# Kernel tuning notes

Measured on AMD Instinct MI355X. Metric: run time of the kernel, lower is better.

## Reference

```python
import jax, jax.numpy as jnp
import numpy as np

N_NODES = 100000
N_EDGES = 1600000
D = 128


def setup_inputs() -> dict:
    key = jax.random.key(0)
    ks = jax.random.split(key, 9)
    inp = {
        "embs": jax.random.normal(ks[0], (N_NODES, D), dtype=jnp.float32),
        "edge_index0": jax.random.randint(ks[1], (2, N_EDGES), 0, N_NODES, dtype=jnp.int64 if jax.config.jax_enable_x64 else jnp.int32),
        "edge_index1": jax.random.randint(ks[2], (2, N_EDGES), 0, N_NODES, dtype=jnp.int64 if jax.config.jax_enable_x64 else jnp.int32),
        "w_l0": jax.random.normal(ks[3], (D, D), dtype=jnp.float32) * (1.0 / np.sqrt(D)),
        "w_r0": jax.random.normal(ks[4], (D, D), dtype=jnp.float32) * (1.0 / np.sqrt(D)),
        "b0": jnp.zeros((D,), dtype=jnp.float32),
        "w_l1": jax.random.normal(ks[5], (D, D), dtype=jnp.float32) * (1.0 / np.sqrt(D)),
        "w_r1": jax.random.normal(ks[6], (D, D), dtype=jnp.float32) * (1.0 / np.sqrt(D)),
        "b1": jnp.zeros((D,), dtype=jnp.float32),
    }
    return inp


def _sage_conv(x, edge_index, w_l, w_r, b):
    # PyG SAGEConv: out[i] = lin_l(mean_{j->i} x[j]) + lin_r(x[i])
    src, dst = edge_index[0], edge_index[1]
    n = x.shape[0]
    msg = jnp.take(x, src, axis=0)                                  # [E, D] gather
    summed = jax.ops.segment_sum(msg, dst, num_segments=n)          # [N, D] scatter-add
    cnt = jax.ops.segment_sum(jnp.ones(src.shape, x.dtype), dst, num_segments=n)
    agg = summed / jnp.maximum(cnt, 1.0)[:, None]                   # mean; 0 for isolated nodes
    return agg @ w_l.T + b + x @ w_r.T


def reference(embs, edge_index0, edge_index1, w_l0, w_r0, b0, w_l1, w_r1, b1):
    # layer 0 (not last): dropout (eval -> identity) + GELU (torch default = exact erf)
    x = _sage_conv(embs, edge_index0, w_l0, w_r0, b0)
    x = jax.nn.gelu(x, approximate=False)
    # layer 1 (last): no dropout / activation
    x = _sage_conv(x, edge_index1, w_l1, w_r1, b1)
    return x
```

## Files before the change

### kernel.cpp

```cpp
#include <hip/hip_runtime.h>
#include <hip/hip_fp16.h>
#include <math.h>

#define D 128
#define SH 9
#define BW (1 << SH)
#define EPT 16

typedef _Float16 half4v __attribute__((ext_vector_type(4)));
typedef _Float16 half8  __attribute__((ext_vector_type(8)));
typedef float    floatx16 __attribute__((ext_vector_type(16)));

__global__ __launch_bounds__(256) void cast_half(
        const float* __restrict__ x, _Float16* __restrict__ y, int n) {
    int i = blockIdx.x * 256 + threadIdx.x;
    int idx = i * 4;
    if (idx >= n) return;
    float4 v = *(const float4*)(x + idx);
    half4v h;
    h[0] = (_Float16)v.x; h[1] = (_Float16)v.y;
    h[2] = (_Float16)v.z; h[3] = (_Float16)v.w;
    *(half4v*)(y + idx) = h;
}

__global__ __launch_bounds__(256) void prep_bswz(
        const float* __restrict__ wl, const float* __restrict__ wr,
        _Float16* __restrict__ B) {
    int idx = blockIdx.x * 256 + threadIdx.x;
    if (idx >= 64 * 512) return;
    int j = idx & 7;
    int lane = (idx >> 3) & 63;
    int f = idx >> 9;
    int ks = f >> 2, cb = f & 3;
    int k = ks * 16 + (lane >> 5) * 8 + j;
    int c = cb * 32 + (lane & 31);
    float v = (k < 128) ? wl[c * 128 + k] : wr[c * 128 + (k - 128)];
    B[idx] = (_Float16)v;
}

__global__ __launch_bounds__(256) void hist_coarse(
        const int* __restrict__ ei0, const int* __restrict__ ei1,
        int E, int NBK, int* __restrict__ ccnt) {
    __shared__ int h[512];
    int NBIN = 2 * NBK;
    int t = threadIdx.x;
    h[t] = 0; h[t + 256] = 0;
    __syncthreads();
    int t0 = blockIdx.x * (256 * EPT) + t;
#pragma unroll
    for (int k = 0; k < EPT; ++k) {
        int idx = t0 + k * 256;
        if (idx < 2 * E) {
            int g = idx >= E;
            int e = idx - g * E;
            int dst = (g ? ei1 : ei0)[E + e];
            atomicAdd(&h[g * NBK + (dst >> SH)], 1);
        }
    }
    __syncthreads();
    for (int b = t; b < NBIN; b += 256)
        if (h[b]) atomicAdd(&ccnt[b * 16], h[b]);
}

__global__ __launch_bounds__(256) void scan_coarse(
        const int* __restrict__ ccnt, int NBK, int E, int N,
        int* __restrict__ gbase, int* __restrict__ gcur,
        int* __restrict__ rp0, int* __restrict__ rp1) {
    __shared__ int part[256];
    int t = threadIdx.x;
    for (int g = 0; g < 2; ++g) {
        int v = (t < NBK) ? ccnt[(g * NBK + t) * 16] : 0;
        part[t] = v;
        __syncthreads();
        for (int off = 1; off < 256; off <<= 1) {
            int u = (t >= off) ? part[t - off] : 0;
            __syncthreads();
            part[t] += u;
            __syncthreads();
        }
        if (t < NBK) {
            int ex = (t == 0) ? 0 : part[t - 1];
            int b = g * NBK + t;
            gbase[b] = ex;
            gcur[b * 16] = ex;
        }
        __syncthreads();
    }
    if (t == 0) { rp0[N] = E; rp1[N] = E; }
}

__global__ __launch_bounds__(256) void bin_pass1(
        const int* __restrict__ ei0, const int* __restrict__ ei1,
        int E, int NBK, int* __restrict__ gcur,
        int* __restrict__ stage0, int* __restrict__ stage1) {
    __shared__ int cnt[512];
    __shared__ int base[512];
    int NBIN = 2 * NBK;
    int t = threadIdx.x;
    cnt[t] = 0; cnt[t + 256] = 0;
    __syncthreads();
    int t0 = blockIdx.x * (256 * EPT) + t;
    int pk[EPT];
    int bn[EPT];
#pragma unroll
    for (int k = 0; k < EPT; ++k) {
        int idx = t0 + k * 256;
        bn[k] = -1;
        if (idx < 2 * E) {
            int g = idx >= E;
            int e = idx - g * E;
            const int* ei = g ? ei1 : ei0;
            int src = ei[e];
            int dst = ei[E + e];
            pk[k] = src | ((dst & (BW - 1)) << 17);
            bn[k] = g * NBK + (dst >> SH);
            atomicAdd(&cnt[bn[k]], 1);
        }
    }
    __syncthreads();
    for (int b = t; b < NBIN; b += 256) {
        int c = cnt[b];
        base[b] = c ? atomicAdd(&gcur[b * 16], c) : 0;
        cnt[b] = 0;
    }
    __syncthreads();
#pragma unroll
    for (int k = 0; k < EPT; ++k) {
        if (bn[k] >= 0) {
            int b = bn[k];
            int r = atomicAdd(&cnt[b], 1);
            int* stage = (b >= NBK) ? stage1 : stage0;
            stage[base[b] + r] = pk[k];
        }
    }
}

__global__ __launch_bounds__(256) void bin_pass2(
        const int* __restrict__ gbase,
        const int* __restrict__ stage0, const int* __restrict__ stage1,
        int* __restrict__ rp0, int* __restrict__ rp1,
        int* __restrict__ es0, int* __restrict__ es1,
        int N, int NBK, int E) {
    __shared__ int cnt[BW];
    __shared__ int part[256];
    int b = blockIdx.x;
    int g = b >= NBK;
    int bk = b - g * NBK;
    const int* stage = g ? stage1 : stage0;
    int* rp = g ? rp1 : rp0;
    int* es = g ? es1 : es0;
    int lo = bk << SH;
    int hi = min(lo + BW, N);
    int nd = hi - lo;
    int beg = gbase[b];
    int end = (bk == NBK - 1) ? E : gbase[b + 1];
    int t = threadIdx.x;
    cnt[t] = 0; cnt[t + 256] = 0;
    __syncthreads();
    for (int i = beg + t; i < end; i += 256)
        atomicAdd(&cnt[(unsigned)stage[i] >> 17], 1);
    __syncthreads();
    int c0 = cnt[t * 2], c1 = cnt[t * 2 + 1];
    part[t] = c0 + c1;
    __syncthreads();
    for (int off = 1; off < 256; off <<= 1) {
        int u = (t >= off) ? part[t - off] : 0;
        __syncthreads();
        part[t] += u;
        __syncthreads();
    }
    int ex = (t == 0) ? 0 : part[t - 1];
    int base0 = beg + ex;
    if (t * 2 < nd)     rp[lo + t * 2]     = base0;
    if (t * 2 + 1 < nd) rp[lo + t * 2 + 1] = base0 + c0;
    __syncthreads();
    cnt[t * 2] = base0;
    cnt[t * 2 + 1] = base0 + c0;
    __syncthreads();
    int i = beg + t;
    for (; i + 768 < end; i += 1024) {
        unsigned p0 = (unsigned)stage[i];
        unsigned p1 = (unsigned)stage[i + 256];
        unsigned p2 = (unsigned)stage[i + 512];
        unsigned p3 = (unsigned)stage[i + 768];
        int q0 = atomicAdd(&cnt[p0 >> 17], 1);
        int q1 = atomicAdd(&cnt[p1 >> 17], 1);
        int q2 = atomicAdd(&cnt[p2 >> 17], 1);
        int q3 = atomicAdd(&cnt[p3 >> 17], 1);
        es[q0] = p0 & 0x1FFFF;
        es[q1] = p1 & 0x1FFFF;
        es[q2] = p2 & 0x1FFFF;
        es[q3] = p3 & 0x1FFFF;
    }
    for (; i < end; i += 256) {
        unsigned p = (unsigned)stage[i];
        int q = atomicAdd(&cnt[p >> 17], 1);
        es[q] = p & 0x1FFFF;
    }
}

__global__ __launch_bounds__(256) void agg_half(
        const _Float16* __restrict__ x, const int* __restrict__ row_ptr,
        const int* __restrict__ edge_src, _Float16* __restrict__ agg, int N) {
    int gt = blockIdx.x * 256 + threadIdx.x;
    int w = gt >> 6;
    int lane = gt & 63;
    if (w >= N) return;
    int beg = row_ptr[w];
    int end = row_ptr[w + 1];
    int grp = lane >> 5;
    int c   = lane & 31;
    unsigned co = (unsigned)c * 8u;
    const char* xb = (const char*)x;
    float ax = 0.f, ay = 0.f, az = 0.f, aw = 0.f;
    float one = 1.0f;

    for (int chunk = beg; chunk < end; chunk += 64) {
        int n = min(64, end - chunk);
        int iv = (lane < n) ? edge_src[chunk + lane] : -1;
        for (int e = 0; e < n; e += 8) {
            int s[4];
            uint2 v[4];
#pragma unroll
            for (int j = 0; j < 4; ++j)
                s[j] = __shfl(iv, e + 2 * j + grp);
#pragma unroll
            for (int j = 0; j < 4; ++j) {
                v[j] = make_uint2(0u, 0u);
                if (s[j] >= 0)
                    v[j] = *(const uint2*)(xb + (unsigned)s[j] * 256u + co);
            }
#pragma unroll
            for (int j = 0; j < 4; ++j) {
                asm("v_fma_mix_f32 %0, %1, %2, %0 op_sel:[0,0,0] op_sel_hi:[1,0,0]"
                    : "+v"(ax) : "v"(v[j].x), "v"(one));
                asm("v_fma_mix_f32 %0, %1, %2, %0 op_sel:[1,0,0] op_sel_hi:[1,0,0]"
                    : "+v"(ay) : "v"(v[j].x), "v"(one));
                asm("v_fma_mix_f32 %0, %1, %2, %0 op_sel:[0,0,0] op_sel_hi:[1,0,0]"
                    : "+v"(az) : "v"(v[j].y), "v"(one));
                asm("v_fma_mix_f32 %0, %1, %2, %0 op_sel:[1,0,0] op_sel_hi:[1,0,0]"
                    : "+v"(aw) : "v"(v[j].y), "v"(one));
            }
        }
    }

    ax += __shfl_xor(ax, 32);
    ay += __shfl_xor(ay, 32);
    az += __shfl_xor(az, 32);
    aw += __shfl_xor(aw, 32);

    int deg = end - beg;
    float inv = (deg > 0) ? 1.0f / (float)deg : 0.0f;
    if (lane < 32) {
        half4v h;
        h[0] = (_Float16)(ax * inv);
        h[1] = (_Float16)(ay * inv);
        h[2] = (_Float16)(az * inv);
        h[3] = (_Float16)(aw * inv);
        *(half4v*)((char*)agg + (size_t)w * 256 + co) = h;
    }
}

__device__ __forceinline__ float gelu_fast(float v) {
    float z = v * 0.70710678118654752f;
    float s = fabsf(z);
    float t = __builtin_amdgcn_rcpf(fmaf(0.3275911f, s, 1.0f));
    float poly = t * fmaf(t, fmaf(t, fmaf(t, fmaf(t, 1.061405429f,
                      -1.453152027f), 1.421413741f), -0.284496736f),
                      0.254829592f);
    float e = __builtin_amdgcn_exp2f(-1.4426950408889634f * s * s);
    float erfv = copysignf(fmaf(-poly, e, 1.0f), z);
    return 0.5f * v * (1.0f + erfv);
}

template <bool GELU, typename OutT>
__global__ __launch_bounds__(256) void sage_mfma(
        const _Float16* __restrict__ aggh, const _Float16* __restrict__ xh,
        const _Float16* __restrict__ Bswz, const float* __restrict__ bias,
        OutT* __restrict__ out, int N) {
    __shared__ _Float16 a_lds[256 * 132];

    const int tid = threadIdx.x;
    const int n0 = blockIdx.x * 128;
    const int wave = tid >> 6;
    const int lane = tid & 63;
    const int l31 = lane & 31;
    const int lhi = lane >> 5;

    floatx16 acc[4];
#pragma unroll
    for (int cb = 0; cb < 4; ++cb)
#pragma unroll
        for (int r = 0; r < 16; ++r) acc[cb][r] = 0.0f;

    {
        int isX = tid >> 7;
        int rr = tid & 127;
        const _Float16* src = isX ? xh : aggh;
        _Float16* dstp = a_lds + tid * 132;
        int gn = n0 + rr;
        if (gn < N) {
            const float4* gp = (const float4*)(src + (size_t)gn * 128);
#pragma unroll
            for (int j = 0; j < 16; ++j) {
                float4 v = gp[j];
                float2* w2 = (float2*)(dstp + j * 8);
                w2[0] = make_float2(v.x, v.y);
                w2[1] = make_float2(v.z, v.w);
            }
        } else {
#pragma unroll
            for (int j = 0; j < 16; ++j) {
                float2* w2 = (float2*)(dstp + j * 8);
                w2[0] = make_float2(0.f, 0.f);
                w2[1] = make_float2(0.f, 0.f);
            }
        }
    }
    __syncthreads();

#pragma unroll
    for (int phase = 0; phase < 2; ++phase) {
        const _Float16* ap = a_lds + (phase * 128 + wave * 32 + l31) * 132
                             + lhi * 8;
        const _Float16* bbase = Bswz + ((size_t)phase * 8 * 4 * 512) + lane * 8;
#pragma unroll
        for (int ks = 0; ks < 8; ++ks) {
            half4v alo = *(const half4v*)(ap + ks * 16);
            half4v ahi = *(const half4v*)(ap + ks * 16 + 4);
            half8 afrag = __builtin_shufflevector(alo, ahi, 0, 1, 2, 3, 4, 5, 6, 7);
#pragma unroll
            for (int cb = 0; cb < 4; ++cb) {
                half8 bfrag = *(const half8*)(bbase + (ks * 4 + cb) * 512);
                acc[cb] = __builtin_amdgcn_mfma_f32_32x32x16_f16(
                    afrag, bfrag, acc[cb], 0, 0, 0);
            }
        }
    }

#pragma unroll
    for (int cb = 0; cb < 4; ++cb) {
        int col = cb * 32 + l31;
        float bv = bias[col];
#pragma unroll
        for (int r = 0; r < 16; ++r) {
            int rowin = (r & 3) + 8 * (r >> 2) + 4 * lhi;
            int grow = n0 + wave * 32 + rowin;
            if (grow < N) {
                float v = acc[cb][r] + bv;
                if (GELU) v = gelu_fast(v);
                out[(size_t)grow * 128 + col] = (OutT)v;
            }
        }
    }
}

extern "C" void kernel_launch(void* const* d_in, const int* in_sizes, int n_in,
                              void* d_out, int out_size, void* d_ws, size_t ws_size,
                              hipStream_t stream) {
    const float* embs = (const float*)d_in[0];
    const int*   ei0  = (const int*)d_in[1];
    const int*   ei1  = (const int*)d_in[2];
    const float* w_l0 = (const float*)d_in[3];
    const float* w_r0 = (const float*)d_in[4];
    const float* b0   = (const float*)d_in[5];
    const float* w_l1 = (const float*)d_in[6];
    const float* w_r1 = (const float*)d_in[7];
    const float* b1   = (const float*)d_in[8];
    float* out = (float*)d_out;

    const int N = in_sizes[0] / D;
    const int E = in_sizes[1] / 2;
    const int NBK = (N + BW - 1) >> SH;
    const int NBIN = 2 * NBK;

    _Float16* x_h   = (_Float16*)d_ws;
    _Float16* h_h   = x_h + (size_t)N * D;
    _Float16* agg_h = h_h + (size_t)N * D;
    _Float16* Bswz0 = agg_h + (size_t)N * D;
    _Float16* Bswz1 = Bswz0 + 64 * 512;
    int* rp0   = (int*)(Bswz1 + 64 * 512);
    int* rp1   = rp0 + (N + 1);
    int* es0   = rp1 + (N + 1);
    int* es1   = es0 + E;
    int* ccnt  = es1 + E;
    int* gbase = ccnt + NBIN * 16;
    int* gcur  = gbase + NBIN;
    int* stage0 = (int*)agg_h;
    int* stage1 = stage0 + E;

    const int cast_grid = ((size_t)N * D / 4 + 255) / 256;
    const int bin_grid  = (2 * E + 256 * EPT - 1) / (256 * EPT);
    const int agg_grid  = ((size_t)N * 64 + 255) / 256;
    const int gemm_grid = (N + 127) / 128;

    cast_half<<<cast_grid, 256, 0, stream>>>(embs, x_h, N * D);
    prep_bswz<<<128, 256, 0, stream>>>(w_l0, w_r0, Bswz0);
    prep_bswz<<<128, 256, 0, stream>>>(w_l1, w_r1, Bswz1);

    hipMemsetAsync(ccnt, 0, (size_t)NBIN * 16 * sizeof(int), stream);
    hist_coarse<<<bin_grid, 256, 0, stream>>>(ei0, ei1, E, NBK, ccnt);
    scan_coarse<<<1, 256, 0, stream>>>(ccnt, NBK, E, N, gbase, gcur, rp0, rp1);
    bin_pass1<<<bin_grid, 256, 0, stream>>>(ei0, ei1, E, NBK, gcur,
                                            stage0, stage1);
    bin_pass2<<<NBIN, 256, 0, stream>>>(gbase, stage0, stage1,
                                        rp0, rp1, es0, es1, N, NBK, E);

    agg_half<<<agg_grid, 256, 0, stream>>>(x_h, rp0, es0, agg_h, N);
    sage_mfma<true, _Float16><<<gemm_grid, 256, 0, stream>>>(
        agg_h, x_h, Bswz0, b0, h_h, N);

    agg_half<<<agg_grid, 256, 0, stream>>>(h_h, rp1, es1, agg_h, N);
    sage_mfma<false, float><<<gemm_grid, 256, 0, stream>>>(
        agg_h, h_h, Bswz1, b1, out, N);
}
```

Before: 414.2 us.

## Preload B fragments into registers with a 2x2 wave tiling in SAGE GEMM

Re-tiles the per-block 128x128 output across four waves as a 2x2 grid, so each wave computes two 32-row blocks by two 32-column blocks instead of one row block by four column blocks. Each wave now loads only its half of the swizzled weight matrix, once into registers, before the LDS barrier. This overlaps the global weight loads with the LDS staging and halves per-wave weight traffic. In exchange each A fragment is read from LDS twice, the 32 half8 weight registers raise VGPR pressure, and launch_bounds asks for 2 blocks per CU.

```diff
diff --git a/kernel.cpp b/kernel.cpp
--- a/kernel.cpp
+++ b/kernel.cpp
@@ -274,7 +274,7 @@
 }
 
 template <bool GELU, typename OutT>
-__global__ __launch_bounds__(256) void sage_mfma(
+__global__ __launch_bounds__(256, 2) void sage_mfma(
         const _Float16* __restrict__ aggh, const _Float16* __restrict__ xh,
         const _Float16* __restrict__ Bswz, const float* __restrict__ bias,
         OutT* __restrict__ out, int N) {
@@ -286,12 +286,19 @@
     const int lane = tid & 63;
     const int l31 = lane & 31;
     const int lhi = lane >> 5;
-
-    floatx16 acc[4];
-#pragma unroll
-    for (int cb = 0; cb < 4; ++cb)
-#pragma unroll
-        for (int r = 0; r < 16; ++r) acc[cb][r] = 0.0f;
+    const int wr = wave >> 1;
+    const int wc = wave & 1;
+
+    half8 breg[2][8][2];
+#pragma unroll
+    for (int ph = 0; ph < 2; ++ph)
+#pragma unroll
+        for (int ks = 0; ks < 8; ++ks)
+#pragma unroll
+            for (int c2 = 0; c2 < 2; ++c2)
+                breg[ph][ks][c2] = *(const half8*)(
+                    Bswz + (size_t)ph * 16384
+                         + ((ks * 4) + (wc * 2 + c2)) * 512 + lane * 8);
 
     {
         int isX = tid >> 7;
@@ -317,42 +324,53 @@
             }
         }
     }
-    __syncthreads();
-
-#pragma unroll
-    for (int phase = 0; phase < 2; ++phase) {
-        const _Float16* ap = a_lds + (phase * 128 + wave * 32 + l31) * 132
-                             + lhi * 8;
-        const _Float16* bbase = Bswz + ((size_t)phase * 8 * 4 * 512) + lane * 8;
-#pragma unroll
-        for (int ks = 0; ks < 8; ++ks) {
-            half4v alo = *(const half4v*)(ap + ks * 16);
-            half4v ahi = *(const half4v*)(ap + ks * 16 + 4);
-            half8 afrag = __builtin_shufflevector(alo, ahi, 0, 1, 2, 3, 4, 5, 6, 7);
-#pragma unroll
-            for (int cb = 0; cb < 4; ++cb) {
-                half8 bfrag = *(const half8*)(bbase + (ks * 4 + cb) * 512);
-                acc[cb] = __builtin_amdgcn_mfma_f32_32x32x16_f16(
-                    afrag, bfrag, acc[cb], 0, 0, 0);
-            }
-        }
-    }
-
-#pragma unroll
-    for (int cb = 0; cb < 4; ++cb) {
-        int col = cb * 32 + l31;
-        float bv = bias[col];
-#pragma unroll
-        for (int r = 0; r < 16; ++r) {
-            int rowin = (r & 3) + 8 * (r >> 2) + 4 * lhi;
-            int grow = n0 + wave * 32 + rowin;
-            if (grow < N) {
-                float v = acc[cb][r] + bv;
-                if (GELU) v = gelu_fast(v);
-                out[(size_t)grow * 128 + col] = (OutT)v;
-            }
-        }
-    }
+
+    floatx16 acc[2][2];
+#pragma unroll
+    for (int r2 = 0; r2 < 2; ++r2)
+#pragma unroll
+        for (int c2 = 0; c2 < 2; ++c2)
+#pragma unroll
+            for (int r = 0; r < 16; ++r) acc[r2][c2][r] = 0.0f;
+
+    __syncthreads();
+
+#pragma unroll
+    for (int ph = 0; ph < 2; ++ph)
+#pragma unroll
+        for (int ks = 0; ks < 8; ++ks)
+#pragma unroll
+            for (int r2 = 0; r2 < 2; ++r2) {
+                const _Float16* ap = a_lds
+                    + (ph * 128 + (wr * 2 + r2) * 32 + l31) * 132
+                    + ks * 16 + lhi * 8;
+                half4v alo = *(const half4v*)(ap);
+                half4v ahi = *(const half4v*)(ap + 4);
+                half8 af = __builtin_shufflevector(alo, ahi,
+                                                   0, 1, 2, 3, 4, 5, 6, 7);
+                acc[r2][0] = __builtin_amdgcn_mfma_f32_32x32x16_f16(
+                    af, breg[ph][ks][0], acc[r2][0], 0, 0, 0);
+                acc[r2][1] = __builtin_amdgcn_mfma_f32_32x32x16_f16(
+                    af, breg[ph][ks][1], acc[r2][1], 0, 0, 0);
+            }
+
+#pragma unroll
+    for (int r2 = 0; r2 < 2; ++r2)
+#pragma unroll
+        for (int c2 = 0; c2 < 2; ++c2) {
+            int col = (wc * 2 + c2) * 32 + l31;
+            float bv = bias[col];
+#pragma unroll
+            for (int r = 0; r < 16; ++r) {
+                int rowin = (r & 3) + 8 * (r >> 2) + 4 * lhi;
+                int grow = n0 + (wr * 2 + r2) * 32 + rowin;
+                if (grow < N) {
+                    float v = acc[r2][c2][r] + bv;
+                    if (GELU) v = gelu_fast(v);
+                    out[(size_t)grow * 128 + col] = (OutT)v;
+                }
+            }
+        }
 }
 
 extern "C" void kernel_launch(void* const* d_in, const int* in_sizes, int n_in,
```

New measurement: 396.5 us. 1.04x faster.
